# Kernel tuning notes

Measured on AMD Instinct MI355X. Metric: run time of the kernel, lower is better.

## Reference

```python
import jax, jax.numpy as jnp
import numpy as np

H = 64   # LSTM hidden size
NL = 8   # LSTM layers
B, T = 2048, 64


def setup_inputs() -> dict:
    key = jax.random.key(0)
    ks = jax.random.split(key, 18)
    r = lambda i, shape, s=0.1: jax.random.normal(ks[i], shape, dtype=jnp.float32) * s
    return {
        "x": r(0, (B, T, 2), 1.0),
        "w1": r(1, (16, 2)), "b1": r(2, (16,)),
        "w2": r(3, (16, 16)), "b2": r(4, (16,)),
        "w_ih0": r(5, (4 * H, 16)), "w_hh0": r(6, (4 * H, H)),
        "b_ih0": r(7, (4 * H,)), "b_hh0": r(8, (4 * H,)),
        "w_ih": r(9, (NL - 1, 4 * H, H)), "w_hh": r(10, (NL - 1, 4 * H, H)),
        "b_ih": r(11, (NL - 1, 4 * H)), "b_hh": r(12, (NL - 1, 4 * H)),
        "wo1": r(13, (32, H)), "bo1": r(14, (32,)),
        "wo2": r(15, (4, 32)), "bo2": r(16, (4,)),
    }


def _lstm_layer(x, w_ih, w_hh, b):
    # x: [B, T, I]; torch gate order: i, f, g, o
    bsz = x.shape[0]
    xg = jnp.einsum('bti,gi->btg', x, w_ih) + b  # [B, T, 4H] precomputed input gates

    def step(carry, xg_t):
        h, c = carry
        gates = xg_t + h @ w_hh.T
        i, f, g, o = jnp.split(gates, 4, axis=-1)
        i = jax.nn.sigmoid(i); f = jax.nn.sigmoid(f)
        g = jnp.tanh(g); o = jax.nn.sigmoid(o)
        c = f * c + i * g
        h = o * jnp.tanh(c)
        return (h, c), h

    h0 = jnp.zeros((bsz, H), x.dtype)
    _, hs = jax.lax.scan(step, (h0, h0), jnp.swapaxes(xg, 0, 1))  # [T, B, H]
    return jnp.swapaxes(hs, 0, 1)


def reference(x, w1, b1, w2, b2, w_ih0, w_hh0, b_ih0, b_hh0,
              w_ih, w_hh, b_ih, b_hh, wo1, bo1, wo2, bo2):
    # action-input MLP: 2 -> 16 -> relu -> 16
    h = jax.nn.relu(x @ w1.T + b1) @ w2.T + b2
    # 8-layer LSTM, hidden 64
    h = _lstm_layer(h, w_ih0, w_hh0, b_ih0 + b_hh0)
    for l in range(NL - 1):
        h = _lstm_layer(h, w_ih[l], w_hh[l], b_ih[l] + b_hh[l])
    # output MLP: 64 -> 32 -> relu -> 4
    return jax.nn.relu(h @ wo1.T + bo1) @ wo2.T + bo2
```

## Files before the change

### kernel.cpp

```cpp
#include <hip/hip_runtime.h>


#define BATCH 2048
#define TT 64
#define HH 64
#define RS 72

typedef short bf16x8 __attribute__((ext_vector_type(8)));
typedef float f32x4 __attribute__((ext_vector_type(4)));

__device__ __forceinline__ float sigmoid_fast(float x) {
    return __builtin_amdgcn_rcpf(1.f + __expf(-x));
}
__device__ __forceinline__ float tanh_fast(float x) {
    float e = __expf(-2.f * x);
    e = fminf(e, 1e30f);
    return (1.f - e) * __builtin_amdgcn_rcpf(1.f + e);
}
__device__ __forceinline__ void split2(float x, unsigned short& hi, unsigned short& lo) {
    const unsigned u = __float_as_uint(x);
    hi = (unsigned short)(u >> 16);
    const float r = x - __uint_as_float(u & 0xFFFF0000u);
    lo = (unsigned short)(__float_as_uint(r) >> 16);
}
__device__ __forceinline__ void wg_wait(int* c, int v) {
    while (__hip_atomic_load(c, __ATOMIC_ACQUIRE, __HIP_MEMORY_SCOPE_WORKGROUP) < v) {}
}
__device__ __forceinline__ void wg_bump(int* c, int lane) {
    if (lane == 0)
        __hip_atomic_fetch_add(c, 1, __ATOMIC_RELEASE, __HIP_MEMORY_SCOPE_WORKGROUP);
}

__global__ __launch_bounds__(256)
void mlp_in_kernel(const float* __restrict__ x,
                   const float* __restrict__ w1, const float* __restrict__ b1,
                   const float* __restrict__ w2, const float* __restrict__ b2,
                   float* __restrict__ out) {
    const int gid = blockIdx.x * 256 + threadIdx.x;
    const float x0 = x[gid * 2 + 0];
    const float x1 = x[gid * 2 + 1];
    float hid[16];
#pragma unroll
    for (int j = 0; j < 16; ++j) {
        float v = fmaf(x1, w1[j * 2 + 1], fmaf(x0, w1[j * 2 + 0], b1[j]));
        hid[j] = fmaxf(0.f, v);
    }
    float o[16];
#pragma unroll
    for (int oo = 0; oo < 16; ++oo) {
        float acc = b2[oo];
#pragma unroll
        for (int j = 0; j < 16; ++j) acc = fmaf(hid[j], w2[oo * 16 + j], acc);
        o[oo] = acc;
    }
    float4* op = (float4*)(out + gid * 16);
#pragma unroll
    for (int q = 0; q < 4; ++q) {
        float4 v;
        v.x = o[q * 4 + 0]; v.y = o[q * 4 + 1]; v.z = o[q * 4 + 2]; v.w = o[q * 4 + 3];
        op[q] = v;
    }
}

template <int IA, int IPADA>
__global__ __launch_bounds__(512, 2)
void lstm_pair(const float* __restrict__ xmlp,
               unsigned* __restrict__ P,
               float* __restrict__ houtf,
               const int last,
               const float* __restrict__ wihA, const float* __restrict__ whhA,
               const float* __restrict__ biA, const float* __restrict__ bhA,
               const float* __restrict__ wihB, const float* __restrict__ whhB,
               const float* __restrict__ biB, const float* __restrict__ bhB) {
    constexpr int KTA = (IPADA + 64) / 32;
    constexpr int KTX = IPADA / 32;
    constexpr int LDPA = IPADA + 8;
    __shared__ __align__(16) unsigned short pAh[2][16 * LDPA], pAl[2][16 * LDPA];
    __shared__ __align__(16) unsigned short rHh[4][16 * RS], rHl[4][16 * RS];
    __shared__ __align__(16) unsigned short pHh[2][16 * RS], pHl[2][16 * RS];
    __shared__ int cA, cB, cBm;

    const int tid = threadIdx.x;
    const int wv = tid >> 6, lane = tid & 63, l16 = lane & 15, quad = lane >> 4;
    const int grp = wv >> 2;
    const int wg = wv & 3;
    const int base = blockIdx.x * 8;
    const bool lo32 = (lane < 32);
    const int bpi = (lane & 31) << 2;

    if (tid == 0) { cA = 0; cB = 0; cBm = 0; }
    for (int e = tid; e < 2 * 16 * LDPA; e += 512) { (&pAh[0][0])[e] = 0; (&pAl[0][0])[e] = 0; }
    for (int e = tid; e < 4 * 16 * RS; e += 512)   { (&rHh[0][0])[e] = 0; (&rHl[0][0])[e] = 0; }
    for (int e = tid; e < 2 * 16 * RS; e += 512)   { (&pHh[0][0])[e] = 0; (&pHl[0][0])[e] = 0; }

    const int I    = grp ? 64 : IA;
    const int IPAD = grp ? 64 : IPADA;
    const int KT   = grp ? 4  : KTA;
    const float* wih = grp ? wihB : wihA;
    const float* whh = grp ? whhB : whhA;
    const float* bi  = grp ? biB  : biA;
    const float* bh  = grp ? bhB  : bhA;

    const int jg = 16 * wg + l16;
    bf16x8 bhi[4][4], blo[4][4];
    float bsum[4];
#pragma unroll
    for (int gt = 0; gt < 4; ++gt) {
        const int n = gt * 64 + jg;
        bsum[gt] = bi[n] + bh[n];
#pragma unroll
        for (int kt = 0; kt < 4; ++kt) {
            bf16x8 vh = {0, 0, 0, 0, 0, 0, 0, 0};
            bf16x8 vl = {0, 0, 0, 0, 0, 0, 0, 0};
            if (kt < KT) {
#pragma unroll
                for (int j = 0; j < 8; ++j) {
                    const int k = kt * 32 + quad * 8 + j;
                    float w = 0.f;
                    if (k < I) w = wih[n * I + k];
                    else if (k >= IPAD) w = whh[n * 64 + (k - IPAD)];
                    unsigned short h_, l_;
                    split2(w, h_, l_);
                    vh[j] = (short)h_;
                    vl[j] = (short)l_;
                }
            }
            bhi[kt][gt] = vh;
            blo[kt][gt] = vl;
        }
    }

    float cs[2] = {0.f, 0.f};
    const int row0 = (quad & 1) * 4 + ((quad >> 1) << 1);

    float2 xr2 = {0.f, 0.f};
    uint2 xru = {0u, 0u};
    int sr = 0, sc = 0, srd = 0;
    bool stg = false;
    if (grp == 0) {
        if (IA == 16) {
            stg = (tid < 128);
            sr = tid >> 3; sc = (tid & 7) * 2;
            srd = base + (sr & 7);
            if (stg) {
                xr2 = *(const float2*)&xmlp[((size_t)srd * TT + 0) * 16 + sc];
                unsigned short h0, l0, h1, l1;
                split2(xr2.x, h0, l0); split2(xr2.y, h1, l1);
                *(unsigned*)&pAh[0][sr * LDPA + sc] = ((unsigned)h1 << 16) | h0;
                *(unsigned*)&pAl[0][sr * LDPA + sc] = ((unsigned)l1 << 16) | l0;
                xr2 = *(const float2*)&xmlp[((size_t)srd * TT + 1) * 16 + sc];
            }
        } else {
            stg = true;
            sr = tid >> 5; sc = (tid & 31) * 2;
            srd = base + sr;
            xru = *(const uint2*)&P[((size_t)srd * TT + 0) * 64 + sc];
            *(unsigned*)&pAh[0][sr * LDPA + sc] = (xru.y & 0xFFFF0000u) | (xru.x >> 16);
            *(unsigned*)&pAl[0][sr * LDPA + sc] = (xru.y << 16) | (xru.x & 0xFFFFu);
            xru = *(const uint2*)&P[((size_t)srd * TT + 1) * 64 + sc];
        }
    }
    __syncthreads();

    if (grp == 0) {
        for (int t = 0; t < TT; ++t) {
            const int pb = t & 1;
            const int rsl = t & 3;
            const int rpr = (t + 3) & 3;
            if (t) wg_wait(&cA, 4 * t);
            if (stg) {
                if (IA == 16) {
                    unsigned short h0, l0, h1, l1;
                    split2(xr2.x, h0, l0); split2(xr2.y, h1, l1);
                    *(unsigned*)&pAh[pb ^ 1][sr * LDPA + sc] = ((unsigned)h1 << 16) | h0;
                    *(unsigned*)&pAl[pb ^ 1][sr * LDPA + sc] = ((unsigned)l1 << 16) | l0;
                    const int tp = (t + 2) & (TT - 1);
                    xr2 = *(const float2*)&xmlp[((size_t)srd * TT + tp) * 16 + sc];
                } else {
                    *(unsigned*)&pAh[pb ^ 1][sr * LDPA + sc] = (xru.y & 0xFFFF0000u) | (xru.x >> 16);
                    *(unsigned*)&pAl[pb ^ 1][sr * LDPA + sc] = (xru.y << 16) | (xru.x & 0xFFFFu);
                    const int tp = (t + 2) & (TT - 1);
                    xru = *(const uint2*)&P[((size_t)srd * TT + tp) * 64 + sc];
                }
            }
            bf16x8 ahi[4], alo[4];
#pragma unroll
            for (int kt = 0; kt < KTA; ++kt) {
                if (kt < KTX) {
                    const int aoff = l16 * LDPA + kt * 32 + quad * 8;
                    ahi[kt] = *(const bf16x8*)&pAh[pb][aoff];
                    alo[kt] = *(const bf16x8*)&pAl[pb][aoff];
                } else {
                    const int aoff = l16 * RS + (kt - KTX) * 32 + quad * 8;
                    ahi[kt] = *(const bf16x8*)&rHh[rpr][aoff];
                    alo[kt] = *(const bf16x8*)&rHl[rpr][aoff];
                }
            }
            f32x4 a0[4], a1[4], a2[4];
#pragma unroll
            for (int gt = 0; gt < 4; ++gt) {
                a0[gt][0] = bsum[gt]; a0[gt][1] = bsum[gt];
                a0[gt][2] = bsum[gt]; a0[gt][3] = bsum[gt];
                a1[gt] = (f32x4){0.f, 0.f, 0.f, 0.f};
                a2[gt] = (f32x4){0.f, 0.f, 0.f, 0.f};
            }
            __builtin_amdgcn_s_setprio(1);
#pragma unroll
            for (int kt = 0; kt < KTA; ++kt) {
#pragma unroll
                for (int gt = 0; gt < 4; ++gt) {
                    a0[gt] = __builtin_amdgcn_mfma_f32_16x16x32_bf16(ahi[kt], bhi[kt][gt], a0[gt], 0, 0, 0);
                    a1[gt] = __builtin_amdgcn_mfma_f32_16x16x32_bf16(alo[kt], bhi[kt][gt], a1[gt], 0, 0, 0);
                    a2[gt] = __builtin_amdgcn_mfma_f32_16x16x32_bf16(ahi[kt], blo[kt][gt], a2[gt], 0, 0, 0);
                }
            }
            __builtin_amdgcn_s_setprio(0);
            f32x4 s4[4];
#pragma unroll
            for (int gt = 0; gt < 4; ++gt) s4[gt] = (a0[gt] + a1[gt]) + a2[gt];
            float gk[4][2];
#pragma unroll
            for (int gt = 0; gt < 4; ++gt) {
#pragma unroll
                for (int r = 0; r < 2; ++r) {
                    const float up = __uint_as_float(
                        __builtin_amdgcn_ds_bpermute(bpi, __float_as_uint(s4[gt][r + 2])));
                    gk[gt][r] = lo32 ? s4[gt][r] : up;
                }
            }
            float hv[2];
#pragma unroll
            for (int r = 0; r < 2; ++r) {
                const float iv = sigmoid_fast(gk[0][r]);
                const float fv = sigmoid_fast(gk[1][r]);
                const float gv = tanh_fast(gk[2][r]);
                const float ov = sigmoid_fast(gk[3][r]);
                const float cn = fv * cs[r] + iv * gv;
                cs[r] = cn;
                hv[r] = ov * tanh_fast(cn);
            }
            if (t >= 4) wg_wait(&cBm, 4 * (t - 3));
#pragma unroll
            for (int r = 0; r < 2; ++r) {
                const int R = row0 + r;
                unsigned short h_, l_;
                split2(hv[r], h_, l_);
                rHh[rsl][R * RS + jg] = h_;
                rHl[rsl][R * RS + jg] = l_;
            }
            wg_bump(&cA, lane);
        }
    } else {
        for (int t = 0; t < TT; ++t) {
            const int pb = t & 1;
            const int rsl = t & 3;
            if (t) wg_wait(&cB, 4 * t);
            wg_wait(&cA, 4 * (t + 1));
            bf16x8 ahi[4], alo[4];
#pragma unroll
            for (int kt = 0; kt < 2; ++kt) {
                const int aoff = l16 * RS + kt * 32 + quad * 8;
                ahi[kt] = *(const bf16x8*)&rHh[rsl][aoff];
                alo[kt] = *(const bf16x8*)&rHl[rsl][aoff];
            }
#pragma unroll
            for (int kt = 2; kt < 4; ++kt) {
                const int aoff = l16 * RS + (kt - 2) * 32 + quad * 8;
                ahi[kt] = *(const bf16x8*)&pHh[pb ^ 1][aoff];
                alo[kt] = *(const bf16x8*)&pHl[pb ^ 1][aoff];
            }
            wg_bump(&cBm, lane);
            f32x4 a0[4], a1[4], a2[4];
#pragma unroll
            for (int gt = 0; gt < 4; ++gt) {
                a0[gt][0] = bsum[gt]; a0[gt][1] = bsum[gt];
                a0[gt][2] = bsum[gt]; a0[gt][3] = bsum[gt];
                a1[gt] = (f32x4){0.f, 0.f, 0.f, 0.f};
                a2[gt] = (f32x4){0.f, 0.f, 0.f, 0.f};
            }
            __builtin_amdgcn_s_setprio(1);
#pragma unroll
            for (int kt = 0; kt < 4; ++kt) {
#pragma unroll
                for (int gt = 0; gt < 4; ++gt) {
                    a0[gt] = __builtin_amdgcn_mfma_f32_16x16x32_bf16(ahi[kt], bhi[kt][gt], a0[gt], 0, 0, 0);
                    a1[gt] = __builtin_amdgcn_mfma_f32_16x16x32_bf16(alo[kt], bhi[kt][gt], a1[gt], 0, 0, 0);
                    a2[gt] = __builtin_amdgcn_mfma_f32_16x16x32_bf16(ahi[kt], blo[kt][gt], a2[gt], 0, 0, 0);
                }
            }
            __builtin_amdgcn_s_setprio(0);
            f32x4 s4[4];
#pragma unroll
            for (int gt = 0; gt < 4; ++gt) s4[gt] = (a0[gt] + a1[gt]) + a2[gt];
            float gk[4][2];
#pragma unroll
            for (int gt = 0; gt < 4; ++gt) {
#pragma unroll
                for (int r = 0; r < 2; ++r) {
                    const float up = __uint_as_float(
                        __builtin_amdgcn_ds_bpermute(bpi, __float_as_uint(s4[gt][r + 2])));
                    gk[gt][r] = lo32 ? s4[gt][r] : up;
                }
            }
#pragma unroll
            for (int r = 0; r < 2; ++r) {
                const float iv = sigmoid_fast(gk[0][r]);
                const float fv = sigmoid_fast(gk[1][r]);
                const float gv = tanh_fast(gk[2][r]);
                const float ov = sigmoid_fast(gk[3][r]);
                const float cn = fv * cs[r] + iv * gv;
                cs[r] = cn;
                const float h = ov * tanh_fast(cn);
                const int R = row0 + r;
                unsigned short h_, l_;
                split2(h, h_, l_);
                pHh[pb][R * RS + jg] = h_;
                pHl[pb][R * RS + jg] = l_;
                if (!last) {
                    P[((size_t)(base + R) * TT + t) * 64 + jg] =
                        ((unsigned)h_ << 16) | (unsigned)l_;
                } else {
                    houtf[((size_t)(base + R) * TT + t) * HH + jg] = h;
                }
            }
            wg_bump(&cB, lane);
        }
    }
}

__global__ __launch_bounds__(256)
void mlp_out_kernel(const float* __restrict__ hin,
                    const float* __restrict__ wo1, const float* __restrict__ bo1,
                    const float* __restrict__ wo2, const float* __restrict__ bo2,
                    float* __restrict__ out) {
    __shared__ __align__(16) float wo1_s[32 * 64];
    __shared__ float bo1_s[32];
    __shared__ float wo2_s[4 * 32];
    __shared__ float bo2_s[4];
    const int tid = threadIdx.x;
    for (int e = tid; e < 32 * 64; e += 256) wo1_s[e] = wo1[e];
    if (tid < 32) bo1_s[tid] = bo1[tid];
    if (tid < 128) wo2_s[tid] = wo2[tid];
    if (tid < 4) bo2_s[tid] = bo2[tid];
    __syncthreads();

    const int gid = blockIdx.x * 256 + tid;
    const float4* hv = (const float4*)(hin + gid * 64);
    float4 h[16];
#pragma unroll
    for (int q = 0; q < 16; ++q) h[q] = hv[q];

    float m1[32];
#pragma unroll
    for (int o = 0; o < 32; ++o) {
        float acc = bo1_s[o];
        const float4* wrow = (const float4*)(wo1_s + o * 64);
#pragma unroll
        for (int q = 0; q < 16; ++q) {
            const float4 w = wrow[q];
            acc = fmaf(h[q].x, w.x, acc);
            acc = fmaf(h[q].y, w.y, acc);
            acc = fmaf(h[q].z, w.z, acc);
            acc = fmaf(h[q].w, w.w, acc);
        }
        m1[o] = fmaxf(0.f, acc);
    }
    float r[4];
#pragma unroll
    for (int q = 0; q < 4; ++q) {
        float acc = bo2_s[q];
#pragma unroll
        for (int o = 0; o < 32; ++o) acc = fmaf(m1[o], wo2_s[q * 32 + o], acc);
        r[q] = acc;
    }
    float4 res;
    res.x = r[0]; res.y = r[1]; res.z = r[2]; res.w = r[3];
    ((float4*)out)[gid] = res;
}

extern "C" void kernel_launch(void* const* d_in, const int* in_sizes, int n_in,
                              void* d_out, int out_size, void* d_ws, size_t ws_size,
                              hipStream_t stream) {
    const float* x     = (const float*)d_in[0];
    const float* w1    = (const float*)d_in[1];
    const float* b1    = (const float*)d_in[2];
    const float* w2    = (const float*)d_in[3];
    const float* b2    = (const float*)d_in[4];
    const float* w_ih0 = (const float*)d_in[5];
    const float* w_hh0 = (const float*)d_in[6];
    const float* b_ih0 = (const float*)d_in[7];
    const float* b_hh0 = (const float*)d_in[8];
    const float* w_ih  = (const float*)d_in[9];
    const float* w_hh  = (const float*)d_in[10];
    const float* b_ih  = (const float*)d_in[11];
    const float* b_hh  = (const float*)d_in[12];
    const float* wo1   = (const float*)d_in[13];
    const float* bo1   = (const float*)d_in[14];
    const float* wo2   = (const float*)d_in[15];
    const float* bo2   = (const float*)d_in[16];

    float* buf_mlp = (float*)d_ws;
    unsigned* P = (unsigned*)(buf_mlp + (size_t)BATCH * TT * 16);
    float* bufH = (float*)(P + (size_t)BATCH * TT * 64);

    const int nbt_blocks = (BATCH * TT) / 256;

    mlp_in_kernel<<<nbt_blocks, 256, 0, stream>>>(x, w1, b1, w2, b2, buf_mlp);

    lstm_pair<16, 32><<<BATCH / 8, 512, 0, stream>>>(
        buf_mlp, P, bufH, 0,
        w_ih0, w_hh0, b_ih0, b_hh0,
        w_ih + (size_t)0 * 256 * 64, w_hh + (size_t)0 * 256 * 64, b_ih + 0 * 256, b_hh + 0 * 256);

    for (int p = 1; p < 4; ++p) {
        const int la = 2 * p - 1, lb = 2 * p;
        lstm_pair<64, 64><<<BATCH / 8, 512, 0, stream>>>(
            buf_mlp, P, bufH, (p == 3) ? 1 : 0,
            w_ih + (size_t)la * 256 * 64, w_hh + (size_t)la * 256 * 64,
            b_ih + la * 256, b_hh + la * 256,
            w_ih + (size_t)lb * 256 * 64, w_hh + (size_t)lb * 256 * 64,
            b_ih + lb * 256, b_hh + lb * 256);
    }

    mlp_out_kernel<<<nbt_blocks, 256, 0, stream>>>(bufH, wo1, bo1, wo2, bo2, (float*)d_out);
}
```

Before: 509.2 us.

## Process 16 batch rows per block, using every row of the MFMA tile

Each LSTM pair block now handles 16 batch rows instead of 8, so all 16 M-rows of the 16x16 MFMA tiles carry real data. This halves the grid size and removes the bpermute shuffle that previously packed 8 rows into half the lanes. Each lane now evaluates gate nonlinearities for 4 rows instead of 2. Staging loads are widened to uint4 (float for the first layer) so all threads take part. The trade-off is fewer blocks (128) on a large GPU, which lowers parallelism across CUs, plus more per-lane elementwise work in each time step.

```diff
diff --git a/kernel.cpp b/kernel.cpp
--- a/kernel.cpp
+++ b/kernel.cpp
@@ -8,6 +8,7 @@
 
 typedef short bf16x8 __attribute__((ext_vector_type(8)));
 typedef float f32x4 __attribute__((ext_vector_type(4)));
+typedef unsigned short u16x4 __attribute__((ext_vector_type(4)));
 
 __device__ __forceinline__ float sigmoid_fast(float x) {
     return __builtin_amdgcn_rcpf(1.f + __expf(-x));
@@ -84,9 +85,7 @@
     const int wv = tid >> 6, lane = tid & 63, l16 = lane & 15, quad = lane >> 4;
     const int grp = wv >> 2;
     const int wg = wv & 3;
-    const int base = blockIdx.x * 8;
-    const bool lo32 = (lane < 32);
-    const int bpi = (lane & 31) << 2;
+    const int base = blockIdx.x * 16;
 
     if (tid == 0) { cA = 0; cB = 0; cBm = 0; }
     for (int e = tid; e < 2 * 16 * LDPA; e += 512) { (&pAh[0][0])[e] = 0; (&pAl[0][0])[e] = 0; }
@@ -130,34 +129,31 @@
         }
     }
 
-    float cs[2] = {0.f, 0.f};
-    const int row0 = (quad & 1) * 4 + ((quad >> 1) << 1);
-
-    float2 xr2 = {0.f, 0.f};
-    uint2 xru = {0u, 0u};
-    int sr = 0, sc = 0, srd = 0;
-    bool stg = false;
+    float cs[4] = {0.f, 0.f, 0.f, 0.f};
+
+    float xrf = 0.f;
+    uint4 xr4 = {0u, 0u, 0u, 0u};
+    const int sr = tid >> 4;
+    const int scf = tid & 15;
+    const int sc4 = (tid & 15) * 4;
     if (grp == 0) {
         if (IA == 16) {
-            stg = (tid < 128);
-            sr = tid >> 3; sc = (tid & 7) * 2;
-            srd = base + (sr & 7);
-            if (stg) {
-                xr2 = *(const float2*)&xmlp[((size_t)srd * TT + 0) * 16 + sc];
-                unsigned short h0, l0, h1, l1;
-                split2(xr2.x, h0, l0); split2(xr2.y, h1, l1);
-                *(unsigned*)&pAh[0][sr * LDPA + sc] = ((unsigned)h1 << 16) | h0;
-                *(unsigned*)&pAl[0][sr * LDPA + sc] = ((unsigned)l1 << 16) | l0;
-                xr2 = *(const float2*)&xmlp[((size_t)srd * TT + 1) * 16 + sc];
-            }
+            xrf = xmlp[((size_t)(base + sr) * TT + 0) * 16 + scf];
+            unsigned short h_, l_;
+            split2(xrf, h_, l_);
+            pAh[0][sr * LDPA + scf] = h_;
+            pAl[0][sr * LDPA + scf] = l_;
+            xrf = xmlp[((size_t)(base + sr) * TT + 1) * 16 + scf];
         } else {
-            stg = true;
-            sr = tid >> 5; sc = (tid & 31) * 2;
-            srd = base + sr;
-            xru = *(const uint2*)&P[((size_t)srd * TT + 0) * 64 + sc];
-            *(unsigned*)&pAh[0][sr * LDPA + sc] = (xru.y & 0xFFFF0000u) | (xru.x >> 16);
-            *(unsigned*)&pAl[0][sr * LDPA + sc] = (xru.y << 16) | (xru.x & 0xFFFFu);
-            xru = *(const uint2*)&P[((size_t)srd * TT + 1) * 64 + sc];
+            xr4 = *(const uint4*)&P[((size_t)(base + sr) * TT + 0) * 64 + sc4];
+            u16x4 hv, lv;
+            hv[0] = (unsigned short)(xr4.x >> 16); lv[0] = (unsigned short)(xr4.x & 0xffffu);
+            hv[1] = (unsigned short)(xr4.y >> 16); lv[1] = (unsigned short)(xr4.y & 0xffffu);
+            hv[2] = (unsigned short)(xr4.z >> 16); lv[2] = (unsigned short)(xr4.z & 0xffffu);
+            hv[3] = (unsigned short)(xr4.w >> 16); lv[3] = (unsigned short)(xr4.w & 0xffffu);
+            *(u16x4*)&pAh[0][sr * LDPA + sc4] = hv;
+            *(u16x4*)&pAl[0][sr * LDPA + sc4] = lv;
+            xr4 = *(const uint4*)&P[((size_t)(base + sr) * TT + 1) * 64 + sc4];
         }
     }
     __syncthreads();
@@ -168,20 +164,23 @@
             const int rsl = t & 3;
             const int rpr = (t + 3) & 3;
             if (t) wg_wait(&cA, 4 * t);
-            if (stg) {
-                if (IA == 16) {
-                    unsigned short h0, l0, h1, l1;
-                    split2(xr2.x, h0, l0); split2(xr2.y, h1, l1);
-                    *(unsigned*)&pAh[pb ^ 1][sr * LDPA + sc] = ((unsigned)h1 << 16) | h0;
-                    *(unsigned*)&pAl[pb ^ 1][sr * LDPA + sc] = ((unsigned)l1 << 16) | l0;
-                    const int tp = (t + 2) & (TT - 1);
-                    xr2 = *(const float2*)&xmlp[((size_t)srd * TT + tp) * 16 + sc];
-                } else {
-                    *(unsigned*)&pAh[pb ^ 1][sr * LDPA + sc] = (xru.y & 0xFFFF0000u) | (xru.x >> 16);
-                    *(unsigned*)&pAl[pb ^ 1][sr * LDPA + sc] = (xru.y << 16) | (xru.x & 0xFFFFu);
-                    const int tp = (t + 2) & (TT - 1);
-                    xru = *(const uint2*)&P[((size_t)srd * TT + tp) * 64 + sc];
-                }
+            if (IA == 16) {
+                unsigned short h_, l_;
+                split2(xrf, h_, l_);
+                pAh[pb ^ 1][sr * LDPA + scf] = h_;
+                pAl[pb ^ 1][sr * LDPA + scf] = l_;
+                const int tp = (t + 2) & (TT - 1);
+                xrf = xmlp[((size_t)(base + sr) * TT + tp) * 16 + scf];
+            } else {
+                u16x4 hv, lv;
+                hv[0] = (unsigned short)(xr4.x >> 16); lv[0] = (unsigned short)(xr4.x & 0xffffu);
+                hv[1] = (unsigned short)(xr4.y >> 16); lv[1] = (unsigned short)(xr4.y & 0xffffu);
+                hv[2] = (unsigned short)(xr4.z >> 16); lv[2] = (unsigned short)(xr4.z & 0xffffu);
+                hv[3] = (unsigned short)(xr4.w >> 16); lv[3] = (unsigned short)(xr4.w & 0xffffu);
+                *(u16x4*)&pAh[pb ^ 1][sr * LDPA + sc4] = hv;
+                *(u16x4*)&pAl[pb ^ 1][sr * LDPA + sc4] = lv;
+                const int tp = (t + 2) & (TT - 1);
+                xr4 = *(const uint4*)&P[((size_t)(base + sr) * TT + tp) * 64 + sc4];
             }
             bf16x8 ahi[4], alo[4];
 #pragma unroll
@@ -218,33 +217,23 @@
             f32x4 s4[4];
 #pragma unroll
             for (int gt = 0; gt < 4; ++gt) s4[gt] = (a0[gt] + a1[gt]) + a2[gt];
-            float gk[4][2];
-#pragma unroll
-            for (int gt = 0; gt < 4; ++gt) {
-#pragma unroll
-                for (int r = 0; r < 2; ++r) {
-                    const float up = __uint_as_float(
-                        __builtin_amdgcn_ds_bpermute(bpi, __float_as_uint(s4[gt][r + 2])));
-                    gk[gt][r] = lo32 ? s4[gt][r] : up;
-                }
-            }
-            float hv[2];
-#pragma unroll
-            for (int r = 0; r < 2; ++r) {
-                const float iv = sigmoid_fast(gk[0][r]);
-                const float fv = sigmoid_fast(gk[1][r]);
-                const float gv = tanh_fast(gk[2][r]);
-                const float ov = sigmoid_fast(gk[3][r]);
-                const float cn = fv * cs[r] + iv * gv;
-                cs[r] = cn;
-                hv[r] = ov * tanh_fast(cn);
+            float hv4[4];
+#pragma unroll
+            for (int rr = 0; rr < 4; ++rr) {
+                const float iv = sigmoid_fast(s4[0][rr]);
+                const float fv = sigmoid_fast(s4[1][rr]);
+                const float gv = tanh_fast(s4[2][rr]);
+                const float ov = sigmoid_fast(s4[3][rr]);
+                const float cn = fv * cs[rr] + iv * gv;
+                cs[rr] = cn;
+                hv4[rr] = ov * tanh_fast(cn);
             }
             if (t >= 4) wg_wait(&cBm, 4 * (t - 3));
 #pragma unroll
-            for (int r = 0; r < 2; ++r) {
-                const int R = row0 + r;
+            for (int rr = 0; rr < 4; ++rr) {
+                const int R = quad * 4 + rr;
                 unsigned short h_, l_;
-                split2(hv[r], h_, l_);
+                split2(hv4[rr], h_, l_);
                 rHh[rsl][R * RS + jg] = h_;
                 rHl[rsl][R * RS + jg] = l_;
             }
@@ -292,26 +281,16 @@
             f32x4 s4[4];
 #pragma unroll
             for (int gt = 0; gt < 4; ++gt) s4[gt] = (a0[gt] + a1[gt]) + a2[gt];
-            float gk[4][2];
-#pragma unroll
-            for (int gt = 0; gt < 4; ++gt) {
-#pragma unroll
-                for (int r = 0; r < 2; ++r) {
-                    const float up = __uint_as_float(
-                        __builtin_amdgcn_ds_bpermute(bpi, __float_as_uint(s4[gt][r + 2])));
-                    gk[gt][r] = lo32 ? s4[gt][r] : up;
-                }
-            }
-#pragma unroll
-            for (int r = 0; r < 2; ++r) {
-                const float iv = sigmoid_fast(gk[0][r]);
-                const float fv = sigmoid_fast(gk[1][r]);
-                const float gv = tanh_fast(gk[2][r]);
-                const float ov = sigmoid_fast(gk[3][r]);
-                const float cn = fv * cs[r] + iv * gv;
-                cs[r] = cn;
+#pragma unroll
+            for (int rr = 0; rr < 4; ++rr) {
+                const float iv = sigmoid_fast(s4[0][rr]);
+                const float fv = sigmoid_fast(s4[1][rr]);
+                const float gv = tanh_fast(s4[2][rr]);
+                const float ov = sigmoid_fast(s4[3][rr]);
+                const float cn = fv * cs[rr] + iv * gv;
+                cs[rr] = cn;
                 const float h = ov * tanh_fast(cn);
-                const int R = row0 + r;
+                const int R = quad * 4 + rr;
                 unsigned short h_, l_;
                 split2(h, h_, l_);
                 pHh[pb][R * RS + jg] = h_;
@@ -407,14 +386,14 @@
 
     mlp_in_kernel<<<nbt_blocks, 256, 0, stream>>>(x, w1, b1, w2, b2, buf_mlp);
 
-    lstm_pair<16, 32><<<BATCH / 8, 512, 0, stream>>>(
+    lstm_pair<16, 32><<<BATCH / 16, 512, 0, stream>>>(
         buf_mlp, P, bufH, 0,
         w_ih0, w_hh0, b_ih0, b_hh0,
         w_ih + (size_t)0 * 256 * 64, w_hh + (size_t)0 * 256 * 64, b_ih + 0 * 256, b_hh + 0 * 256);
 
     for (int p = 1; p < 4; ++p) {
         const int la = 2 * p - 1, lb = 2 * p;
-        lstm_pair<64, 64><<<BATCH / 8, 512, 0, stream>>>(
+        lstm_pair<64, 64><<<BATCH / 16, 512, 0, stream>>>(
             buf_mlp, P, bufH, (p == 3) ? 1 : 0,
             w_ih + (size_t)la * 256 * 64, w_hh + (size_t)la * 256 * 64,
             b_ih + la * 256, b_hh + la * 256,
```

New measurement: 608.7 us. +19.6%, slower.

## Issue input-projection MFMAs before waiting on recurrent state; deepen input buffer ring

Applied to the files above, without the earlier changes.

In the first layer group, the input-part MFMAs now run before the wait on the previous step's hidden state, and only the recurrent part runs after the wait. This moves independent work off the serial critical path. The input staging buffer goes from two to four slots so staging can write two steps ahead without racing readers that no longer sit behind the barrier. In the second group, the loads of its own previous hidden state are hoisted above the wait on layer A. The cost is more shared memory (which may affect occupancy) and more complex slot indexing.

```diff
diff --git a/kernel.cpp b/kernel.cpp
--- a/kernel.cpp
+++ b/kernel.cpp
@@ -75,7 +75,7 @@
     constexpr int KTA = (IPADA + 64) / 32;
     constexpr int KTX = IPADA / 32;
     constexpr int LDPA = IPADA + 8;
-    __shared__ __align__(16) unsigned short pAh[2][16 * LDPA], pAl[2][16 * LDPA];
+    __shared__ __align__(16) unsigned short pAh[4][16 * LDPA], pAl[4][16 * LDPA];
     __shared__ __align__(16) unsigned short rHh[4][16 * RS], rHl[4][16 * RS];
     __shared__ __align__(16) unsigned short pHh[2][16 * RS], pHl[2][16 * RS];
     __shared__ int cA, cB, cBm;
@@ -89,7 +89,7 @@
     const int bpi = (lane & 31) << 2;
 
     if (tid == 0) { cA = 0; cB = 0; cBm = 0; }
-    for (int e = tid; e < 2 * 16 * LDPA; e += 512) { (&pAh[0][0])[e] = 0; (&pAl[0][0])[e] = 0; }
+    for (int e = tid; e < 4 * 16 * LDPA; e += 512) { (&pAh[0][0])[e] = 0; (&pAl[0][0])[e] = 0; }
     for (int e = tid; e < 4 * 16 * RS; e += 512)   { (&rHh[0][0])[e] = 0; (&rHl[0][0])[e] = 0; }
     for (int e = tid; e < 2 * 16 * RS; e += 512)   { (&pHh[0][0])[e] = 0; (&pHl[0][0])[e] = 0; }
 
@@ -143,59 +143,37 @@
             sr = tid >> 3; sc = (tid & 7) * 2;
             srd = base + (sr & 7);
             if (stg) {
-                xr2 = *(const float2*)&xmlp[((size_t)srd * TT + 0) * 16 + sc];
-                unsigned short h0, l0, h1, l1;
-                split2(xr2.x, h0, l0); split2(xr2.y, h1, l1);
-                *(unsigned*)&pAh[0][sr * LDPA + sc] = ((unsigned)h1 << 16) | h0;
-                *(unsigned*)&pAl[0][sr * LDPA + sc] = ((unsigned)l1 << 16) | l0;
-                xr2 = *(const float2*)&xmlp[((size_t)srd * TT + 1) * 16 + sc];
+#pragma unroll
+                for (int s = 0; s < 2; ++s) {
+                    xr2 = *(const float2*)&xmlp[((size_t)srd * TT + s) * 16 + sc];
+                    unsigned short h0, l0, h1, l1;
+                    split2(xr2.x, h0, l0); split2(xr2.y, h1, l1);
+                    *(unsigned*)&pAh[s][sr * LDPA + sc] = ((unsigned)h1 << 16) | h0;
+                    *(unsigned*)&pAl[s][sr * LDPA + sc] = ((unsigned)l1 << 16) | l0;
+                }
+                xr2 = *(const float2*)&xmlp[((size_t)srd * TT + 2) * 16 + sc];
             }
         } else {
             stg = true;
             sr = tid >> 5; sc = (tid & 31) * 2;
             srd = base + sr;
-            xru = *(const uint2*)&P[((size_t)srd * TT + 0) * 64 + sc];
-            *(unsigned*)&pAh[0][sr * LDPA + sc] = (xru.y & 0xFFFF0000u) | (xru.x >> 16);
-            *(unsigned*)&pAl[0][sr * LDPA + sc] = (xru.y << 16) | (xru.x & 0xFFFFu);
-            xru = *(const uint2*)&P[((size_t)srd * TT + 1) * 64 + sc];
+#pragma unroll
+            for (int s = 0; s < 2; ++s) {
+                xru = *(const uint2*)&P[((size_t)srd * TT + s) * 64 + sc];
+                *(unsigned*)&pAh[s][sr * LDPA + sc] = (xru.y & 0xFFFF0000u) | (xru.x >> 16);
+                *(unsigned*)&pAl[s][sr * LDPA + sc] = (xru.y << 16) | (xru.x & 0xFFFFu);
+            }
+            xru = *(const uint2*)&P[((size_t)srd * TT + 2) * 64 + sc];
         }
     }
     __syncthreads();
 
     if (grp == 0) {
         for (int t = 0; t < TT; ++t) {
-            const int pb = t & 1;
+            const int xsl = t & 3;
             const int rsl = t & 3;
             const int rpr = (t + 3) & 3;
-            if (t) wg_wait(&cA, 4 * t);
-            if (stg) {
-                if (IA == 16) {
-                    unsigned short h0, l0, h1, l1;
-                    split2(xr2.x, h0, l0); split2(xr2.y, h1, l1);
-                    *(unsigned*)&pAh[pb ^ 1][sr * LDPA + sc] = ((unsigned)h1 << 16) | h0;
-                    *(unsigned*)&pAl[pb ^ 1][sr * LDPA + sc] = ((unsigned)l1 << 16) | l0;
-                    const int tp = (t + 2) & (TT - 1);
-                    xr2 = *(const float2*)&xmlp[((size_t)srd * TT + tp) * 16 + sc];
-                } else {
-                    *(unsigned*)&pAh[pb ^ 1][sr * LDPA + sc] = (xru.y & 0xFFFF0000u) | (xru.x >> 16);
-                    *(unsigned*)&pAl[pb ^ 1][sr * LDPA + sc] = (xru.y << 16) | (xru.x & 0xFFFFu);
-                    const int tp = (t + 2) & (TT - 1);
-                    xru = *(const uint2*)&P[((size_t)srd * TT + tp) * 64 + sc];
-                }
-            }
-            bf16x8 ahi[4], alo[4];
-#pragma unroll
-            for (int kt = 0; kt < KTA; ++kt) {
-                if (kt < KTX) {
-                    const int aoff = l16 * LDPA + kt * 32 + quad * 8;
-                    ahi[kt] = *(const bf16x8*)&pAh[pb][aoff];
-                    alo[kt] = *(const bf16x8*)&pAl[pb][aoff];
-                } else {
-                    const int aoff = l16 * RS + (kt - KTX) * 32 + quad * 8;
-                    ahi[kt] = *(const bf16x8*)&rHh[rpr][aoff];
-                    alo[kt] = *(const bf16x8*)&rHl[rpr][aoff];
-                }
-            }
+
             f32x4 a0[4], a1[4], a2[4];
 #pragma unroll
             for (int gt = 0; gt < 4; ++gt) {
@@ -204,17 +182,65 @@
                 a1[gt] = (f32x4){0.f, 0.f, 0.f, 0.f};
                 a2[gt] = (f32x4){0.f, 0.f, 0.f, 0.f};
             }
-            __builtin_amdgcn_s_setprio(1);
-#pragma unroll
-            for (int kt = 0; kt < KTA; ++kt) {
-#pragma unroll
-                for (int gt = 0; gt < 4; ++gt) {
-                    a0[gt] = __builtin_amdgcn_mfma_f32_16x16x32_bf16(ahi[kt], bhi[kt][gt], a0[gt], 0, 0, 0);
-                    a1[gt] = __builtin_amdgcn_mfma_f32_16x16x32_bf16(alo[kt], bhi[kt][gt], a1[gt], 0, 0, 0);
-                    a2[gt] = __builtin_amdgcn_mfma_f32_16x16x32_bf16(ahi[kt], blo[kt][gt], a2[gt], 0, 0, 0);
-                }
-            }
-            __builtin_amdgcn_s_setprio(0);
+            {
+                bf16x8 xhi[KTX], xlo[KTX];
+#pragma unroll
+                for (int kt = 0; kt < KTX; ++kt) {
+                    const int aoff = l16 * LDPA + kt * 32 + quad * 8;
+                    xhi[kt] = *(const bf16x8*)&pAh[xsl][aoff];
+                    xlo[kt] = *(const bf16x8*)&pAl[xsl][aoff];
+                }
+                __builtin_amdgcn_s_setprio(1);
+#pragma unroll
+                for (int kt = 0; kt < KTX; ++kt) {
+#pragma unroll
+                    for (int gt = 0; gt < 4; ++gt) {
+                        a0[gt] = __builtin_amdgcn_mfma_f32_16x16x32_bf16(xhi[kt], bhi[kt][gt], a0[gt], 0, 0, 0);
+                        a1[gt] = __builtin_amdgcn_mfma_f32_16x16x32_bf16(xlo[kt], bhi[kt][gt], a1[gt], 0, 0, 0);
+                        a2[gt] = __builtin_amdgcn_mfma_f32_16x16x32_bf16(xhi[kt], blo[kt][gt], a2[gt], 0, 0, 0);
+                    }
+                }
+                __builtin_amdgcn_s_setprio(0);
+            }
+            if (stg) {
+                const int wsl = (t + 2) & 3;
+                if (IA == 16) {
+                    unsigned short h0, l0, h1, l1;
+                    split2(xr2.x, h0, l0); split2(xr2.y, h1, l1);
+                    *(unsigned*)&pAh[wsl][sr * LDPA + sc] = ((unsigned)h1 << 16) | h0;
+                    *(unsigned*)&pAl[wsl][sr * LDPA + sc] = ((unsigned)l1 << 16) | l0;
+                    const int tp = (t + 3) & (TT - 1);
+                    xr2 = *(const float2*)&xmlp[((size_t)srd * TT + tp) * 16 + sc];
+                } else {
+                    *(unsigned*)&pAh[wsl][sr * LDPA + sc] = (xru.y & 0xFFFF0000u) | (xru.x >> 16);
+                    *(unsigned*)&pAl[wsl][sr * LDPA + sc] = (xru.y << 16) | (xru.x & 0xFFFFu);
+                    const int tp = (t + 3) & (TT - 1);
+                    xru = *(const uint2*)&P[((size_t)srd * TT + tp) * 64 + sc];
+                }
+            }
+
+            if (t) wg_wait(&cA, 4 * t);
+            {
+                bf16x8 hhi[KTA - KTX], hlo[KTA - KTX];
+#pragma unroll
+                for (int kt = KTX; kt < KTA; ++kt) {
+                    const int aoff = l16 * RS + (kt - KTX) * 32 + quad * 8;
+                    hhi[kt - KTX] = *(const bf16x8*)&rHh[rpr][aoff];
+                    hlo[kt - KTX] = *(const bf16x8*)&rHl[rpr][aoff];
+                }
+                __builtin_amdgcn_s_setprio(1);
+#pragma unroll
+                for (int kt = KTX; kt < KTA; ++kt) {
+#pragma unroll
+                    for (int gt = 0; gt < 4; ++gt) {
+                        a0[gt] = __builtin_amdgcn_mfma_f32_16x16x32_bf16(hhi[kt - KTX], bhi[kt][gt], a0[gt], 0, 0, 0);
+                        a1[gt] = __builtin_amdgcn_mfma_f32_16x16x32_bf16(hlo[kt - KTX], bhi[kt][gt], a1[gt], 0, 0, 0);
+                        a2[gt] = __builtin_amdgcn_mfma_f32_16x16x32_bf16(hhi[kt - KTX], blo[kt][gt], a2[gt], 0, 0, 0);
+                    }
+                }
+                __builtin_amdgcn_s_setprio(0);
+            }
+
             f32x4 s4[4];
 #pragma unroll
             for (int gt = 0; gt < 4; ++gt) s4[gt] = (a0[gt] + a1[gt]) + a2[gt];
@@ -255,19 +281,19 @@
             const int pb = t & 1;
             const int rsl = t & 3;
             if (t) wg_wait(&cB, 4 * t);
+            bf16x8 ahi[4], alo[4];
+#pragma unroll
+            for (int kt = 2; kt < 4; ++kt) {
+                const int aoff = l16 * RS + (kt - 2) * 32 + quad * 8;
+                ahi[kt] = *(const bf16x8*)&pHh[pb ^ 1][aoff];
+                alo[kt] = *(const bf16x8*)&pHl[pb ^ 1][aoff];
+            }
             wg_wait(&cA, 4 * (t + 1));
-            bf16x8 ahi[4], alo[4];
 #pragma unroll
             for (int kt = 0; kt < 2; ++kt) {
                 const int aoff = l16 * RS + kt * 32 + quad * 8;
                 ahi[kt] = *(const bf16x8*)&rHh[rsl][aoff];
                 alo[kt] = *(const bf16x8*)&rHl[rsl][aoff];
-            }
-#pragma unroll
-            for (int kt = 2; kt < 4; ++kt) {
-                const int aoff = l16 * RS + (kt - 2) * 32 + quad * 8;
-                ahi[kt] = *(const bf16x8*)&pHh[pb ^ 1][aoff];
-                alo[kt] = *(const bf16x8*)&pHl[pb ^ 1][aoff];
             }
             wg_bump(&cBm, lane);
             f32x4 a0[4], a1[4], a2[4];
```

After: 528.1 us. +3.7%, slower.
